# Optimization experiments

Measured on AMD Instinct MI355X. Metric: run time of the kernel, lower is better.

Reference implementation:

```python
import jax, jax.numpy as jnp
import numpy as np

B, D, C = 512, 16384, 3
SAMPLE_DURATION = 16
NEG_THRESHOLD = 0.5
NEGPOS_RATIO = 3


def setup_inputs() -> dict:
    key = jax.random.key(0)
    k1, k2, k3, k4, k5, k6, k7 = jax.random.split(key, 7)
    loc_pred = jax.random.normal(k1, (B, D, 2), dtype=jnp.float32)
    conf_pred = jax.random.normal(k2, (B, D, C), dtype=jnp.float32)
    # one ground-truth (start, end, label) per sample, within [0, 16]
    start = jax.random.uniform(k3, (B,), dtype=jnp.float32) * 8.0
    length = 1.0 + jax.random.uniform(k4, (B,), dtype=jnp.float32) * 7.0
    label = jax.random.randint(k5, (B,), 0, C).astype(jnp.float32)
    targets = jnp.stack([start, start + length, label], axis=-1)  # [B,3]
    # default bars stored as (center, length) in frame units
    centers = 1.0 + jax.random.uniform(k6, (D,), dtype=jnp.float32) * (SAMPLE_DURATION - 2.0)
    lengths = 1.0 + jax.random.uniform(k7, (D,), dtype=jnp.float32) * (SAMPLE_DURATION - 4.0)
    default_bar = jnp.stack([centers, lengths], axis=-1)  # [D,2]
    return {"loc_pred": loc_pred, "conf_pred": conf_pred,
            "targets": targets, "default_bar": default_bar}


def _match_one(truth, label, default):
    """truth [2]=(start,end), label scalar int, default [D,2]=(center,length).
    Returns loc_t [D,2], conf_t [D] (0=ignore, 1=background, >1=fg)."""
    d_c, d_l = default[:, 0], default[:, 1]
    d_s, d_e = d_c - d_l * 0.5, d_c + d_l * 0.5
    inter = jnp.clip(jnp.minimum(truth[1], d_e) - jnp.maximum(truth[0], d_s), 0.0)
    union = (truth[1] - truth[0]) + (d_e - d_s) - inter
    ov = inter / union                                   # [D] 1-D IoU
    best_prior = jnp.argmax(ov)                          # best anchor for the truth
    bto = ov.at[best_prior].set(2.0)                     # index_fill_ with 2
    conf = jnp.full((D,), label + 1, dtype=jnp.int32)    # single truth -> broadcast
    is_bg = conf == 1
    conf = jnp.where(bto < NEG_THRESHOLD, 0, conf)
    conf = jnp.where(is_bg, 1, conf)
    # SSD-style encoding of matched (start,end) against (center,length)
    m_c = (truth[0] + truth[1]) * 0.5
    m_l = truth[1] - truth[0]
    loc = jnp.stack([(m_c - d_c) / d_l, jnp.log(m_l / d_l)], axis=-1)  # [D,2]
    return loc, conf


def reference(loc_pred, conf_pred, targets, default_bar):
    truths = targets[:, :2]                              # [B,2]
    labels = targets[:, 2].astype(jnp.int32)             # [B]
    loc_t, conf_t = jax.vmap(_match_one, in_axes=(0, 0, None))(truths, labels, default_bar)
    loc_t = jax.lax.stop_gradient(loc_t)                 # built under no_grad in torch
    conf_t = jax.lax.stop_gradient(conf_t)

    pos = conf_t > 0                                     # [B,D] used for mining
    loc_pos = conf_t > 1                                 # [B,D] used for loc loss

    # SmoothL1 (beta=1), reduction='sum' over positives
    diff = loc_pred - loc_t
    ad = jnp.abs(diff)
    sl1 = jnp.where(ad < 1.0, 0.5 * diff * diff, ad - 0.5)
    loss_loc = jnp.sum(sl1 * loc_pos[..., None].astype(sl1.dtype))

    # hard-negative mining on per-anchor CE surrogate
    conf_tc = jnp.clip(conf_t - 1, 0)                    # [B,D] class ids 0..C-1
    lse = jax.nn.logsumexp(conf_pred, axis=-1)           # [B,D]
    gathered = jnp.take_along_axis(conf_pred, conf_tc[..., None], axis=-1)[..., 0]
    lc = lse - gathered
    lc = jnp.where(pos, 0.0, lc)
    loss_idx = jnp.argsort(-lc, axis=1)                  # descending sort
    idx_rank = jnp.argsort(loss_idx, axis=1)
    num_pos = jnp.sum(pos.astype(jnp.int32), axis=1, keepdims=True)   # [B,1]
    num_neg = jnp.clip(NEGPOS_RATIO * num_pos, max=D - 1)
    neg = idx_rank < num_neg                             # [B,D]

    sel = (pos | neg).astype(conf_pred.dtype)
    logp = jax.nn.log_softmax(conf_pred, axis=-1)
    ce = -jnp.take_along_axis(logp, conf_tc[..., None], axis=-1)[..., 0]
    loss_conf = jnp.sum(ce * sel)

    N = jnp.sum(num_pos).astype(loss_loc.dtype)
    return jnp.stack([loss_loc / N, loss_conf / N])
```

## Files before the change

kernel.cpp:

```cpp
#include <hip/hip_runtime.h>
#include <hip/hip_fp16.h>
#include <math.h>

constexpr int Bn = 512;
constexpr int Dn = 16384;
constexpr int BS = 512;
constexpr int CHUNKS = 16;
constexpr int CPRI = Dn / CHUNKS;
constexpr int K1T = 256;

__device__ __forceinline__ float lse3(float a, float b, float c) {
  float m = fmaxf(a, fmaxf(b, c));
  return m + __logf(__expf(a - m) + __expf(b - m) + __expf(c - m));
}
__device__ __forceinline__ float sl1f(float x) {
  float a = fabsf(x);
  return a < 1.f ? 0.5f * x * x : a - 0.5f;
}

__device__ __forceinline__ double blockReduceAddD(double v, double* sred) {
  int t = threadIdx.x;
  sred[t] = v;
  __syncthreads();
  for (int off = BS >> 1; off > 0; off >>= 1) {
    if (t < off) sred[t] += sred[t + off];
    __syncthreads();
  }
  double r = sred[0];
  __syncthreads();
  return r;
}

__global__ __launch_bounds__(K1T) void multiloss_stream(
    const float* __restrict__ loc_pred, const float* __restrict__ conf_pred,
    const float* __restrict__ targets, const float* __restrict__ default_bar,
    unsigned* __restrict__ lc32,
    float* __restrict__ pce, float* __restrict__ plloc, int* __restrict__ pnpos)
{
  __shared__ float s_red[12];

  const int bid = blockIdx.x;
  const int b = bid >> 4, c = bid & 15;
  const int t = threadIdx.x;
  const int l = t & 63, w = t >> 6;

  const int p0 = c * CPRI + 4 * t;

  const float4* cp4 = (const float4*)(conf_pred + (size_t)b * Dn * 3 + (size_t)p0 * 3);
  const float4* bp4 = (const float4*)(default_bar + (size_t)p0 * 2);
  float4 C0 = cp4[0], C1 = cp4[1], C2 = cp4[2];
  float4 B0 = bp4[0], B1 = bp4[1];
  __builtin_amdgcn_sched_barrier(0);

  const float t0  = targets[b * 3 + 0];
  const float t1  = targets[b * 3 + 1];
  const int   lab = (int)targets[b * 3 + 2];

  float ce = 0.f, lloc = 0.f; int npos = 0;
  const float m_c = (t0 + t1) * 0.5f;
  const float T   = t1 - t0;

  const float cf[12] = {C0.x, C0.y, C0.z, C0.w, C1.x, C1.y, C1.z, C1.w, C2.x, C2.y, C2.z, C2.w};
  const float bf[8]  = {B0.x, B0.y, B0.z, B0.w, B1.x, B1.y, B1.z, B1.w};

  if (lab == 0) {
    #pragma unroll
    for (int i = 0; i < 4; ++i) {
      float x = cf[3 * i], y = cf[3 * i + 1], z = cf[3 * i + 2];
      float s = __expf(x) + __expf(y) + __expf(z);
      ce += __logf(s) - x;
    }
  } else {
    const float log_ml = __logf(T);
    const float2* __restrict__ lp2 = (const float2*)loc_pred + (size_t)b * Dn;
    float lcv[4];
    #pragma unroll
    for (int i = 0; i < 4; ++i) {
      float x = cf[3 * i], y = cf[3 * i + 1], z = cf[3 * i + 2];
      float dc = bf[2 * i], dl = bf[2 * i + 1];
      float ds = __fmaf_rn(-0.5f, dl, dc);
      float de = __fmaf_rn(0.5f, dl, dc);
      float inter = fmaxf(fminf(t1, de) - fmaxf(t0, ds), 0.f);
      float uni = (T + dl) - inter;
      bool pos = (2.f * inter >= uni);
      float s = __expf(x) + __expf(y) + __expf(z);
      float lse = __logf(s);
      float cl = (lab == 1) ? y : z;
      npos += pos;
      ce += pos ? (lse - cl) : 0.f;
      lcv[i] = pos ? 0.f : (lse - x);
      if (pos) {
        float2 lp = lp2[p0 + i];
        float pd0 = lp.x - __fdividef(m_c - dc, dl);
        float pd1 = (lp.y - log_ml) + __logf(dl);
        lloc += sl1f(pd0) + sl1f(pd1);
      }
    }
    __half2 h0 = __floats2half2_rn(lcv[0], lcv[1]);
    __half2 h1 = __floats2half2_rn(lcv[2], lcv[3]);
    uint2 pk = make_uint2(*reinterpret_cast<unsigned*>(&h0),
                          *reinterpret_cast<unsigned*>(&h1));
    *((uint2*)(lc32 + ((size_t)b * Dn + p0) / 2)) = pk;
  }

  #pragma unroll
  for (int off = 1; off < 64; off <<= 1) {
    ce   += __shfl_xor(ce, off);
    lloc += __shfl_xor(lloc, off);
    npos += __shfl_xor(npos, off);
  }
  if (l == 0) {
    s_red[w * 3 + 0] = ce; s_red[w * 3 + 1] = lloc; s_red[w * 3 + 2] = __int_as_float(npos);
  }
  __syncthreads();
  if (t == 0) {
    float Ce = 0.f, Ll = 0.f; int Np = 0;
    #pragma unroll
    for (int k = 0; k < 4; ++k) {
      Ce += s_red[k * 3 + 0]; Ll += s_red[k * 3 + 1]; Np += __float_as_int(s_red[k * 3 + 2]);
    }
    int pidx = b * CHUNKS + c;
    pce[pidx] = Ce; plloc[pidx] = Ll; pnpos[pidx] = Np;
  }
}

__global__ __launch_bounds__(BS) void multiloss_select(
    const float* __restrict__ loc_pred, const float* __restrict__ conf_pred,
    const float* __restrict__ targets, const float* __restrict__ default_bar,
    const unsigned short* __restrict__ lc16,
    const float* __restrict__ pce, const float* __restrict__ plloc,
    const int* __restrict__ pnpos,
    double* __restrict__ rloc, double* __restrict__ rconf, double* __restrict__ rnp)
{
  __shared__ unsigned short s_lc[Dn];
  __shared__ int      s_hist[256];
  __shared__ double   s_dred[BS];
  __shared__ float    s_fv[BS];
  __shared__ int      s_fi[BS];
  __shared__ unsigned s_wt[8];
  __shared__ unsigned s_sel[2];
  __shared__ double   s_sc[2];
  __shared__ int      s_np;

  const int b = blockIdx.x;
  const int t = threadIdx.x;
  const int lab = (int)targets[b * 3 + 2];

  if (lab == 0) {
    if (t == 0) {
      double ce = 0.0;
      for (int kk = 0; kk < CHUNKS; ++kk) ce += (double)pce[CHUNKS * b + kk];
      rloc[b] = 0.0; rconf[b] = ce; rnp[b] = (double)Dn;
    }
    return;
  }

  const float t0 = targets[b * 3 + 0];
  const float t1 = targets[b * 3 + 1];

  const float4* lcr = (const float4*)(lc16 + (size_t)b * Dn);
  float4* sl4 = (float4*)s_lc;
  #pragma unroll
  for (int j = 0; j < Dn / 8 / BS; ++j) sl4[j * BS + t] = lcr[j * BS + t];
  __syncthreads();

  if (t == 0) {
    double ce = 0.0, ll = 0.0; int np = 0;
    for (int kk = 0; kk < CHUNKS; ++kk) {
      int pi = CHUNKS * b + kk;
      ce += (double)pce[pi]; ll += (double)plloc[pi]; np += pnpos[pi];
    }
    s_sc[0] = ce; s_sc[1] = ll; s_np = np;
  }
  __syncthreads();
  int np = s_np;

  if (np == 0) {
    float bV = -1.f; int bI = 0;
    for (int d = t; d < Dn; d += BS) {
      float2 db = ((const float2*)default_bar)[d];
      float d_s = db.x - db.y * 0.5f;
      float d_e = db.x + db.y * 0.5f;
      float inter = fmaxf(fminf(t1, d_e) - fmaxf(t0, d_s), 0.f);
      float uni = (t1 - t0) + (d_e - d_s) - inter;
      float ov = inter / uni;
      if (ov > bV) { bV = ov; bI = d; }
    }
    s_fv[t] = bV; s_fi[t] = bI;
    __syncthreads();
    for (int off = BS >> 1; off > 0; off >>= 1) {
      if (t < off) {
        float v2 = s_fv[t + off]; int i2 = s_fi[t + off];
        if (v2 > s_fv[t] || (v2 == s_fv[t] && i2 < s_fi[t])) { s_fv[t] = v2; s_fi[t] = i2; }
      }
      __syncthreads();
    }
    if (t == 0) {
      int d = s_fi[0];
      const float* cp = conf_pred + (size_t)b * Dn * 3 + (size_t)d * 3;
      float c0 = cp[0], c1 = cp[1], c2 = cp[2];
      float lse = lse3(c0, c1, c2);
      float cl = (lab == 1) ? c1 : c2;
      float2 db = ((const float2*)default_bar)[d];
      float2 lp = ((const float2*)loc_pred)[(size_t)b * Dn + d];
      float m_c = (t0 + t1) * 0.5f, m_l = t1 - t0;
      float pd0 = lp.x - (m_c - db.x) / db.y;
      float pd1 = lp.y - __logf(m_l / db.y);
      s_sc[0] += (double)(lse - cl);
      s_sc[1] += (double)(sl1f(pd0) + sl1f(pd1));
      s_np = 1;
      s_lc[d] = 0;
    }
    __syncthreads();
    np = s_np;
  }
  const int k = min(3 * np, Dn - 1);

  unsigned prefix = 0;
  int K = k;
  const int lane = t & 63, w = t >> 6;
  for (int r = 0; r < 2; ++r) {
    if (t < 256) s_hist[t] = 0;
    __syncthreads();
    for (int d = t; d < Dn; d += BS) {
      unsigned u = s_lc[d];
      bool ok = (r == 0) || ((u >> 8) == prefix);
      if (ok) {
        unsigned bin = (r == 0) ? (u >> 8) : (u & 0xFFu);
        atomicAdd(&s_hist[bin], 1);
      }
    }
    __syncthreads();
    unsigned psum = (t < 256) ? (unsigned)s_hist[t] : 0u;
    unsigned incl = psum;
    #pragma unroll
    for (int off = 1; off < 64; off <<= 1) {
      unsigned v = __shfl_down(incl, off, 64);
      if (lane + off < 64) incl += v;
    }
    if (lane == 0) s_wt[w] = incl;
    __syncthreads();
    unsigned aboveW = 0;
    for (int w2 = w + 1; w2 < 8; ++w2) aboveW += s_wt[w2];
    const unsigned above = aboveW + (incl - psum);
    if (t < 256 && above < (unsigned)K && (unsigned)K <= above + psum) {
      s_sel[0] = (unsigned)t;
      s_sel[1] = above;
    }
    __syncthreads();
    unsigned selBin = s_sel[0];
    K -= (int)s_sel[1];
    prefix = (r == 0) ? selBin : ((prefix << 8) | selBin);
    __syncthreads();
  }
  const unsigned tb = prefix;

  float    ssum = 0.f;
  unsigned scnt = 0;
  for (int d = t; d < Dn; d += BS) {
    unsigned u = s_lc[d];
    if (u > tb) {
      ssum += __half2float(__ushort_as_half((unsigned short)u));
      scnt++;
    }
  }
  double S = blockReduceAddD((double)ssum, s_dred);
  double C = blockReduceAddD((double)scnt, s_dred);

  if (t == 0) {
    double tval = (double)__half2float(__ushort_as_half((unsigned short)tb));
    double topk = S + ((double)k - C) * tval;
    rloc[b]  = s_sc[1];
    rconf[b] = s_sc[0] + topk;
    rnp[b]   = (double)np;
  }
}

__global__ __launch_bounds__(BS) void multiloss_mono(
    const float* __restrict__ loc_pred, const float* __restrict__ conf_pred,
    const float* __restrict__ targets, const float* __restrict__ default_bar,
    double* __restrict__ rloc, double* __restrict__ rconf, double* __restrict__ rnp)
{
  __shared__ float    s_lc[Dn];
  __shared__ int      s_hist[2048];
  __shared__ unsigned s_scan[BS];
  __shared__ double   s_dred[BS];
  __shared__ unsigned s_sel[2];
  __shared__ double   s_corr[2];
  __shared__ int      s_np;

  const int b = blockIdx.x;
  const int t = threadIdx.x;

  const float t0  = targets[b * 3 + 0];
  const float t1  = targets[b * 3 + 1];
  const int   lab = (int)targets[b * 3 + 2];

  const float* __restrict__ cpb = conf_pred + (size_t)b * Dn * 3;

  if (lab == 0) {
    float ce = 0.f;
    for (int d = t; d < Dn; d += BS) {
      const float* cp = cpb + d * 3;
      ce += lse3(cp[0], cp[1], cp[2]) - cp[0];
    }
    double tot = blockReduceAddD((double)ce, s_dred);
    if (t == 0) { rloc[b] = 0.0; rconf[b] = tot; rnp[b] = (double)Dn; }
    return;
  }

  const float m_c = (t0 + t1) * 0.5f;
  const float m_l = t1 - t0;

  float bestV = -1.f; int bestI = 0;
  int   nposL = 0;
  float cePosL = 0.f;
  float llocL  = 0.f;

  for (int d = t; d < Dn; d += BS) {
    float2 db = ((const float2*)default_bar)[d];
    float d_c = db.x, d_l = db.y;
    float d_s = d_c - d_l * 0.5f;
    float d_e = d_c + d_l * 0.5f;
    float inter = fmaxf(fminf(t1, d_e) - fmaxf(t0, d_s), 0.f);
    float uni = (t1 - t0) + (d_e - d_s) - inter;
    float ov  = inter / uni;

    const float* cp = cpb + d * 3;
    float c0 = cp[0];
    float lse = lse3(cp[0], cp[1], cp[2]);

    if (ov > bestV) { bestV = ov; bestI = d; }

    float lcv;
    if (ov >= 0.5f) {
      nposL++;
      float cl = (lab == 1) ? cp[1] : cp[2];
      cePosL += lse - cl;
      float2 lp = ((const float2*)loc_pred)[(size_t)b * Dn + d];
      float pd0 = lp.x - (m_c - d_c) / d_l;
      float pd1 = lp.y - __logf(m_l / d_l);
      llocL += sl1f(pd0) + sl1f(pd1);
      lcv = 0.f;
    } else {
      lcv = lse - c0;
    }
    s_lc[d] = lcv;
  }

  float* sv = (float*)s_hist;
  int*   si = (int*)(s_hist + BS);
  sv[t] = bestV; si[t] = bestI;
  __syncthreads();
  for (int off = BS >> 1; off > 0; off >>= 1) {
    if (t < off) {
      float v2 = sv[t + off]; int i2 = si[t + off];
      if (v2 > sv[t] || (v2 == sv[t] && i2 < si[t])) { sv[t] = v2; si[t] = i2; }
    }
    __syncthreads();
  }
  float bV = sv[0]; int bI = si[0];
  __syncthreads();

  double nposTot  = blockReduceAddD((double)nposL, s_dred);
  double cePosTot = blockReduceAddD((double)cePosL, s_dred);
  double llocTot  = blockReduceAddD((double)llocL, s_dred);
  int num_pos = (int)(nposTot + 0.5);

  if (t == 0) {
    double cc = 0.0, lcor = 0.0; int np2 = num_pos;
    if (bV < 0.5f) {
      int d = bI;
      const float* cp = cpb + d * 3;
      float lse = lse3(cp[0], cp[1], cp[2]);
      float cl = (lab == 1) ? cp[1] : cp[2];
      cc = (double)(lse - cl);
      float2 db = ((const float2*)default_bar)[d];
      float2 lp = ((const float2*)loc_pred)[(size_t)b * Dn + d];
      float pd0 = lp.x - (m_c - db.x) / db.y;
      float pd1 = lp.y - __logf(m_l / db.y);
      lcor = (double)(sl1f(pd0) + sl1f(pd1));
      np2 += 1;
      s_lc[d] = 0.f;
    }
    s_corr[0] = cc; s_corr[1] = lcor; s_np = np2;
  }
  __syncthreads();
  int np = s_np;
  int k  = min(3 * np, Dn - 1);

  unsigned prefix = 0;
  int K = k;
  for (int r = 0; r < 3; ++r) {
    for (int i = t; i < 2048; i += BS) s_hist[i] = 0;
    __syncthreads();
    for (int d = t; d < Dn; d += BS) {
      unsigned u = __float_as_uint(s_lc[d]);
      bool ok = (r == 0) || (r == 1 ? ((u >> 21) == prefix) : ((u >> 10) == prefix));
      if (ok) {
        unsigned bin = (r == 0) ? (u >> 21)
                     : (r == 1) ? ((u >> 10) & 0x7FFu)
                                : (u & 0x3FFu);
        atomicAdd(&s_hist[bin], 1);
      }
    }
    __syncthreads();
    int nb  = (r == 2) ? 1024 : 2048;
    int per = nb / BS;
    unsigned psum = 0;
    for (int j = 0; j < per; ++j) psum += (unsigned)s_hist[t * per + j];
    s_scan[t] = psum;
    __syncthreads();
    for (int off = 1; off < BS; off <<= 1) {
      unsigned v = (t + off < BS) ? s_scan[t + off] : 0u;
      __syncthreads();
      s_scan[t] += v;
      __syncthreads();
    }
    unsigned above = (t < BS - 1) ? s_scan[t + 1] : 0u;
    if (above < (unsigned)K && (unsigned)K <= above + psum) {
      unsigned cum = above;
      int found = 0;
      for (int j = per - 1; j >= 0; --j) {
        unsigned c = (unsigned)s_hist[t * per + j];
        if (cum + c >= (unsigned)K) { found = j; break; }
        cum += c;
      }
      s_sel[0] = (unsigned)(t * per + found);
      s_sel[1] = cum;
    }
    __syncthreads();
    unsigned selBin = s_sel[0];
    K -= (int)s_sel[1];
    prefix = (r == 0) ? selBin
           : (r == 1) ? ((prefix << 11) | selBin)
                      : ((prefix << 10) | selBin);
    __syncthreads();
  }
  const unsigned tb = prefix;

  float    ssum = 0.f;
  unsigned scnt = 0;
  for (int d = t; d < Dn; d += BS) {
    float v = s_lc[d];
    if (__float_as_uint(v) > tb) { ssum += v; scnt++; }
  }
  double S = blockReduceAddD((double)ssum, s_dred);
  double C = blockReduceAddD((double)scnt, s_dred);

  if (t == 0) {
    double tval = (double)__uint_as_float(tb);
    double topk = S + ((double)k - C) * tval;
    rloc[b]  = llocTot + s_corr[1];
    rconf[b] = cePosTot + s_corr[0] + topk;
    rnp[b]   = (double)s_np;
  }
}

__global__ __launch_bounds__(512) void multiloss_final(
    const double* __restrict__ rloc, const double* __restrict__ rconf,
    const double* __restrict__ rnp, float* __restrict__ out)
{
  __shared__ double s1[512], s2[512], s3[512];
  int t = threadIdx.x;
  s1[t] = rloc[t];
  s2[t] = rconf[t];
  s3[t] = rnp[t];
  __syncthreads();
  for (int off = 256; off > 0; off >>= 1) {
    if (t < off) { s1[t] += s1[t + off]; s2[t] += s2[t + off]; s3[t] += s3[t + off]; }
    __syncthreads();
  }
  if (t == 0) {
    double N = s3[0];
    out[0] = (float)(s1[0] / N);
    out[1] = (float)(s2[0] / N);
  }
}

extern "C" void kernel_launch(void* const* d_in, const int* in_sizes, int n_in,
                              void* d_out, int out_size, void* d_ws, size_t ws_size,
                              hipStream_t stream) {
  const float* loc_pred    = (const float*)d_in[0];
  const float* conf_pred   = (const float*)d_in[1];
  const float* targets     = (const float*)d_in[2];
  const float* default_bar = (const float*)d_in[3];
  float* out = (float*)d_out;
  char* ws = (char*)d_ws;

  constexpr size_t LC_BYTES = (size_t)Bn * Dn * sizeof(unsigned short);
  constexpr size_t P_CNT = (size_t)Bn * CHUNKS;
  size_t off = LC_BYTES;
  float*  pce   = (float*)(ws + off); off += P_CNT * 4;
  float*  plloc = (float*)(ws + off); off += P_CNT * 4;
  int*    pnpos = (int*)(ws + off);   off += P_CNT * 4;
  double* rloc  = (double*)(ws + off); off += Bn * 8;
  double* rconf = (double*)(ws + off); off += Bn * 8;
  double* rnp   = (double*)(ws + off); off += Bn * 8;
  const size_t NEED = off;

  if (ws_size >= NEED) {
    hipLaunchKernelGGL(multiloss_stream, dim3(Bn * CHUNKS), dim3(K1T), 0, stream,
                       loc_pred, conf_pred, targets, default_bar,
                       (unsigned*)ws, pce, plloc, pnpos);
    hipLaunchKernelGGL(multiloss_select, dim3(Bn), dim3(BS), 0, stream,
                       loc_pred, conf_pred, targets, default_bar,
                       (const unsigned short*)ws, pce, plloc, pnpos,
                       rloc, rconf, rnp);
    hipLaunchKernelGGL(multiloss_final, dim3(1), dim3(512), 0, stream,
                       rloc, rconf, rnp, out);
  } else {
    double* mloc  = (double*)ws;
    double* mconf = mloc + Bn;
    double* mnp   = mconf + Bn;
    hipLaunchKernelGGL(multiloss_mono, dim3(Bn), dim3(BS), 0, stream,
                       loc_pred, conf_pred, targets, default_bar, mloc, mconf, mnp);
    hipLaunchKernelGGL(multiloss_final, dim3(1), dim3(512), 0, stream,
                       mloc, mconf, mnp, out);
  }
}
```

Baseline: 57.73 us.

## Simplify stream kernel to pure CE map; move positive matching into select kernel

The first kernel is reduced to a uniform elementwise map that turns conf_pred into fp16 background CE values, two groups of four anchors per thread, with no per-sample branching, default_bar reads or partial reductions. The select kernel now recomputes IoU positives itself, builds a shared-memory list of positive anchors and zeroes their CE slots. It then gathers conf_pred and loc_pred only for those anchors to form the positive CE and localisation loss. Label-0 samples sum their CE from the fp16 buffer instead of fp32 partials, which costs precision, and the per-block partial arrays are gone.

```diff
diff --git a/kernel.cpp b/kernel.cpp
--- a/kernel.cpp
+++ b/kernel.cpp
@@ -5,9 +5,7 @@
 constexpr int Bn = 512;
 constexpr int Dn = 16384;
 constexpr int BS = 512;
-constexpr int CHUNKS = 16;
-constexpr int CPRI = Dn / CHUNKS;
-constexpr int K1T = 256;
+constexpr int K1B = 4096;
 
 __device__ __forceinline__ float lse3(float a, float b, float c) {
   float m = fmaxf(a, fmaxf(b, c));
@@ -31,154 +29,127 @@
   return r;
 }
 
-__global__ __launch_bounds__(K1T) void multiloss_stream(
-    const float* __restrict__ loc_pred, const float* __restrict__ conf_pred,
-    const float* __restrict__ targets, const float* __restrict__ default_bar,
-    unsigned* __restrict__ lc32,
-    float* __restrict__ pce, float* __restrict__ plloc, int* __restrict__ pnpos)
+__device__ __forceinline__ uint2 lc4(const float4& C0, const float4& C1, const float4& C2) {
+  const float cf[12] = {C0.x, C0.y, C0.z, C0.w, C1.x, C1.y, C1.z, C1.w, C2.x, C2.y, C2.z, C2.w};
+  float o[4];
+  #pragma unroll
+  for (int i = 0; i < 4; ++i) {
+    float x = cf[3 * i], y = cf[3 * i + 1], z = cf[3 * i + 2];
+    float s = __expf(x) + __expf(y) + __expf(z);
+    o[i] = __logf(s) - x;
+  }
+  __half2 h0 = __floats2half2_rn(o[0], o[1]);
+  __half2 h1 = __floats2half2_rn(o[2], o[3]);
+  return make_uint2(*reinterpret_cast<unsigned*>(&h0), *reinterpret_cast<unsigned*>(&h1));
+}
+
+__global__ __launch_bounds__(256) void multiloss_map(
+    const float4* __restrict__ conf4, uint2* __restrict__ lc)
 {
-  __shared__ float s_red[12];
-
-  const int bid = blockIdx.x;
-  const int b = bid >> 4, c = bid & 15;
-  const int t = threadIdx.x;
-  const int l = t & 63, w = t >> 6;
-
-  const int p0 = c * CPRI + 4 * t;
-
-  const float4* cp4 = (const float4*)(conf_pred + (size_t)b * Dn * 3 + (size_t)p0 * 3);
-  const float4* bp4 = (const float4*)(default_bar + (size_t)p0 * 2);
-  float4 C0 = cp4[0], C1 = cp4[1], C2 = cp4[2];
-  float4 B0 = bp4[0], B1 = bp4[1];
+  const size_t nth = (size_t)K1B * 256;
+  const size_t i = (size_t)blockIdx.x * 256 + threadIdx.x;
+  const size_t i2 = i + nth;
+  float4 A0 = conf4[3 * i], A1 = conf4[3 * i + 1], A2 = conf4[3 * i + 2];
+  float4 B0 = conf4[3 * i2], B1 = conf4[3 * i2 + 1], B2 = conf4[3 * i2 + 2];
   __builtin_amdgcn_sched_barrier(0);
-
-  const float t0  = targets[b * 3 + 0];
-  const float t1  = targets[b * 3 + 1];
-  const int   lab = (int)targets[b * 3 + 2];
-
-  float ce = 0.f, lloc = 0.f; int npos = 0;
-  const float m_c = (t0 + t1) * 0.5f;
-  const float T   = t1 - t0;
-
-  const float cf[12] = {C0.x, C0.y, C0.z, C0.w, C1.x, C1.y, C1.z, C1.w, C2.x, C2.y, C2.z, C2.w};
-  const float bf[8]  = {B0.x, B0.y, B0.z, B0.w, B1.x, B1.y, B1.z, B1.w};
-
-  if (lab == 0) {
-    #pragma unroll
-    for (int i = 0; i < 4; ++i) {
-      float x = cf[3 * i], y = cf[3 * i + 1], z = cf[3 * i + 2];
-      float s = __expf(x) + __expf(y) + __expf(z);
-      ce += __logf(s) - x;
-    }
-  } else {
-    const float log_ml = __logf(T);
-    const float2* __restrict__ lp2 = (const float2*)loc_pred + (size_t)b * Dn;
-    float lcv[4];
-    #pragma unroll
-    for (int i = 0; i < 4; ++i) {
-      float x = cf[3 * i], y = cf[3 * i + 1], z = cf[3 * i + 2];
-      float dc = bf[2 * i], dl = bf[2 * i + 1];
-      float ds = __fmaf_rn(-0.5f, dl, dc);
-      float de = __fmaf_rn(0.5f, dl, dc);
-      float inter = fmaxf(fminf(t1, de) - fmaxf(t0, ds), 0.f);
-      float uni = (T + dl) - inter;
-      bool pos = (2.f * inter >= uni);
-      float s = __expf(x) + __expf(y) + __expf(z);
-      float lse = __logf(s);
-      float cl = (lab == 1) ? y : z;
-      npos += pos;
-      ce += pos ? (lse - cl) : 0.f;
-      lcv[i] = pos ? 0.f : (lse - x);
-      if (pos) {
-        float2 lp = lp2[p0 + i];
-        float pd0 = lp.x - __fdividef(m_c - dc, dl);
-        float pd1 = (lp.y - log_ml) + __logf(dl);
-        lloc += sl1f(pd0) + sl1f(pd1);
-      }
-    }
-    __half2 h0 = __floats2half2_rn(lcv[0], lcv[1]);
-    __half2 h1 = __floats2half2_rn(lcv[2], lcv[3]);
-    uint2 pk = make_uint2(*reinterpret_cast<unsigned*>(&h0),
-                          *reinterpret_cast<unsigned*>(&h1));
-    *((uint2*)(lc32 + ((size_t)b * Dn + p0) / 2)) = pk;
-  }
-
-  #pragma unroll
-  for (int off = 1; off < 64; off <<= 1) {
-    ce   += __shfl_xor(ce, off);
-    lloc += __shfl_xor(lloc, off);
-    npos += __shfl_xor(npos, off);
-  }
-  if (l == 0) {
-    s_red[w * 3 + 0] = ce; s_red[w * 3 + 1] = lloc; s_red[w * 3 + 2] = __int_as_float(npos);
-  }
-  __syncthreads();
-  if (t == 0) {
-    float Ce = 0.f, Ll = 0.f; int Np = 0;
-    #pragma unroll
-    for (int k = 0; k < 4; ++k) {
-      Ce += s_red[k * 3 + 0]; Ll += s_red[k * 3 + 1]; Np += __float_as_int(s_red[k * 3 + 2]);
-    }
-    int pidx = b * CHUNKS + c;
-    pce[pidx] = Ce; plloc[pidx] = Ll; pnpos[pidx] = Np;
-  }
+  lc[i]  = lc4(A0, A1, A2);
+  lc[i2] = lc4(B0, B1, B2);
 }
 
 __global__ __launch_bounds__(BS) void multiloss_select(
     const float* __restrict__ loc_pred, const float* __restrict__ conf_pred,
     const float* __restrict__ targets, const float* __restrict__ default_bar,
     const unsigned short* __restrict__ lc16,
-    const float* __restrict__ pce, const float* __restrict__ plloc,
-    const int* __restrict__ pnpos,
     double* __restrict__ rloc, double* __restrict__ rconf, double* __restrict__ rnp)
 {
   __shared__ unsigned short s_lc[Dn];
+  __shared__ unsigned short s_plist[Dn];
   __shared__ int      s_hist[256];
   __shared__ double   s_dred[BS];
   __shared__ float    s_fv[BS];
   __shared__ int      s_fi[BS];
   __shared__ unsigned s_wt[8];
   __shared__ unsigned s_sel[2];
-  __shared__ double   s_sc[2];
-  __shared__ int      s_np;
+  __shared__ int      s_cnt;
 
   const int b = blockIdx.x;
   const int t = threadIdx.x;
   const int lab = (int)targets[b * 3 + 2];
 
   if (lab == 0) {
-    if (t == 0) {
-      double ce = 0.0;
-      for (int kk = 0; kk < CHUNKS; ++kk) ce += (double)pce[CHUNKS * b + kk];
-      rloc[b] = 0.0; rconf[b] = ce; rnp[b] = (double)Dn;
-    }
+    const float4* lcr = (const float4*)(lc16 + (size_t)b * Dn);
+    float part = 0.f;
+    #pragma unroll
+    for (int j = 0; j < Dn / 8 / BS; ++j) {
+      float4 v = lcr[j * BS + t];
+      const __half2* hp = (const __half2*)&v;
+      #pragma unroll
+      for (int q = 0; q < 4; ++q) {
+        float2 f = __half22float2(hp[q]);
+        part += f.x + f.y;
+      }
+    }
+    double tot = blockReduceAddD((double)part, s_dred);
+    if (t == 0) { rloc[b] = 0.0; rconf[b] = tot; rnp[b] = (double)Dn; }
     return;
   }
 
   const float t0 = targets[b * 3 + 0];
   const float t1 = targets[b * 3 + 1];
+  const float m_c = (t0 + t1) * 0.5f;
+  const float m_l = t1 - t0;
+  const float T   = m_l;
+  const float2* __restrict__ bar2 = (const float2*)default_bar;
 
   const float4* lcr = (const float4*)(lc16 + (size_t)b * Dn);
   float4* sl4 = (float4*)s_lc;
   #pragma unroll
   for (int j = 0; j < Dn / 8 / BS; ++j) sl4[j * BS + t] = lcr[j * BS + t];
-  __syncthreads();
-
-  if (t == 0) {
-    double ce = 0.0, ll = 0.0; int np = 0;
-    for (int kk = 0; kk < CHUNKS; ++kk) {
-      int pi = CHUNKS * b + kk;
-      ce += (double)pce[pi]; ll += (double)plloc[pi]; np += pnpos[pi];
-    }
-    s_sc[0] = ce; s_sc[1] = ll; s_np = np;
-  }
-  __syncthreads();
-  int np = s_np;
+  if (t == 0) s_cnt = 0;
+  __syncthreads();
+
+  #pragma unroll
+  for (int j = 0; j < Dn / BS; ++j) {
+    int d = j * BS + t;
+    float2 db = bar2[d];
+    float dc = db.x, dl = db.y;
+    float ds = __fmaf_rn(-0.5f, dl, dc);
+    float de = __fmaf_rn(0.5f, dl, dc);
+    float inter = fmaxf(fminf(t1, de) - fmaxf(t0, ds), 0.f);
+    float uni = (T + dl) - inter;
+    if (2.f * inter >= uni) {
+      int slot = atomicAdd(&s_cnt, 1);
+      s_plist[slot] = (unsigned short)d;
+      s_lc[d] = 0;
+    }
+  }
+  __syncthreads();
+  int np = s_cnt;
+
+  double ceL = 0.0, llL = 0.0;
+  {
+    const float* __restrict__ cpb = conf_pred + (size_t)b * Dn * 3;
+    const float2* __restrict__ lp2 = (const float2*)loc_pred + (size_t)b * Dn;
+    for (int j = t; j < np; j += BS) {
+      int d = s_plist[j];
+      float c0 = cpb[3 * d], c1 = cpb[3 * d + 1], c2 = cpb[3 * d + 2];
+      float lse = lse3(c0, c1, c2);
+      float cl = (lab == 1) ? c1 : c2;
+      ceL += (double)(lse - cl);
+      float2 db = bar2[d];
+      float2 lp = lp2[d];
+      float pd0 = lp.x - (m_c - db.x) / db.y;
+      float pd1 = lp.y - __logf(m_l / db.y);
+      llL += (double)(sl1f(pd0) + sl1f(pd1));
+    }
+  }
+  double ce = blockReduceAddD(ceL, s_dred);
+  double ll = blockReduceAddD(llL, s_dred);
 
   if (np == 0) {
     float bV = -1.f; int bI = 0;
     for (int d = t; d < Dn; d += BS) {
-      float2 db = ((const float2*)default_bar)[d];
+      float2 db = bar2[d];
       float d_s = db.x - db.y * 0.5f;
       float d_e = db.x + db.y * 0.5f;
       float inter = fmaxf(fminf(t1, d_e) - fmaxf(t0, d_s), 0.f);
@@ -201,18 +172,18 @@
       float c0 = cp[0], c1 = cp[1], c2 = cp[2];
       float lse = lse3(c0, c1, c2);
       float cl = (lab == 1) ? c1 : c2;
-      float2 db = ((const float2*)default_bar)[d];
+      float2 db = bar2[d];
       float2 lp = ((const float2*)loc_pred)[(size_t)b * Dn + d];
-      float m_c = (t0 + t1) * 0.5f, m_l = t1 - t0;
       float pd0 = lp.x - (m_c - db.x) / db.y;
       float pd1 = lp.y - __logf(m_l / db.y);
-      s_sc[0] += (double)(lse - cl);
-      s_sc[1] += (double)(sl1f(pd0) + sl1f(pd1));
-      s_np = 1;
+      s_dred[0] = ce + (double)(lse - cl);
+      s_dred[1] = ll + (double)(sl1f(pd0) + sl1f(pd1));
       s_lc[d] = 0;
     }
     __syncthreads();
-    np = s_np;
+    ce = s_dred[0]; ll = s_dred[1];
+    np = 1;
+    __syncthreads();
   }
   const int k = min(3 * np, Dn - 1);
 
@@ -270,8 +241,8 @@
   if (t == 0) {
     double tval = (double)__half2float(__ushort_as_half((unsigned short)tb));
     double topk = S + ((double)k - C) * tval;
-    rloc[b]  = s_sc[1];
-    rconf[b] = s_sc[0] + topk;
+    rloc[b]  = ll;
+    rconf[b] = ce + topk;
     rnp[b]   = (double)np;
   }
 }
@@ -489,24 +460,18 @@
   char* ws = (char*)d_ws;
 
   constexpr size_t LC_BYTES = (size_t)Bn * Dn * sizeof(unsigned short);
-  constexpr size_t P_CNT = (size_t)Bn * CHUNKS;
   size_t off = LC_BYTES;
-  float*  pce   = (float*)(ws + off); off += P_CNT * 4;
-  float*  plloc = (float*)(ws + off); off += P_CNT * 4;
-  int*    pnpos = (int*)(ws + off);   off += P_CNT * 4;
   double* rloc  = (double*)(ws + off); off += Bn * 8;
   double* rconf = (double*)(ws + off); off += Bn * 8;
   double* rnp   = (double*)(ws + off); off += Bn * 8;
   const size_t NEED = off;
 
   if (ws_size >= NEED) {
-    hipLaunchKernelGGL(multiloss_stream, dim3(Bn * CHUNKS), dim3(K1T), 0, stream,
-                       loc_pred, conf_pred, targets, default_bar,
-                       (unsigned*)ws, pce, plloc, pnpos);
+    hipLaunchKernelGGL(multiloss_map, dim3(K1B), dim3(256), 0, stream,
+                       (const float4*)conf_pred, (uint2*)ws);
     hipLaunchKernelGGL(multiloss_select, dim3(Bn), dim3(BS), 0, stream,
                        loc_pred, conf_pred, targets, default_bar,
-                       (const unsigned short*)ws, pce, plloc, pnpos,
-                       rloc, rconf, rnp);
+                       (const unsigned short*)ws, rloc, rconf, rnp);
     hipLaunchKernelGGL(multiloss_final, dim3(1), dim3(512), 0, stream,
                        rloc, rconf, rnp, out);
   } else {
```

Result: slower. 75.39 us (+30.6%).
